# Optimization experiments

Measured on AMD Instinct MI355X. Metric: run time of the kernel, lower is better.

## Reference

```python
import jax, jax.numpy as jnp
import numpy as np

B = 32768   # batch (agents)
D = 2       # data_dim
E = 16      # embedding_dim
H = 128     # h_dim
M = 6       # num_modes
T = 30      # pred_len
EPS = 1e-5  # GroupNorm eps


def gn(x, w, b):
    # GroupNorm with 1 group over the last (channel) axis, per sample
    mu = x.mean(-1, keepdims=True)
    var = x.var(-1, keepdims=True)
    return (x - mu) * jax.lax.rsqrt(var + EPS) * w + b


def setup_inputs() -> dict:
    key = jax.random.key(0)
    ks = jax.random.split(key, 24)
    def n(k, shp, s=0.08):
        return jax.random.normal(k, shp, jnp.float32) * s
    return dict(
        last_obs=jax.random.normal(ks[0], (B, D), jnp.float32),
        last_obs_rel=jax.random.normal(ks[1], (B, D), jnp.float32),
        h0=jax.random.normal(ks[2], (B, H), jnp.float32),
        c0=jax.random.normal(ks[3], (B, H), jnp.float32),
        W_se=n(ks[4], (E, M * D)), b_se=n(ks[5], (E,)),
        W_ih=n(ks[6], (4 * H, E)), W_hh=n(ks[7], (4 * H, H)),
        b_ih=n(ks[8], (4 * H,)), b_hh=n(ks[9], (4 * H,)),
        mW1=n(ks[10], (M, H, H)), mg1w=jnp.ones((M, H)), mg1b=jnp.zeros((M, H)),
        mW2=n(ks[11], (M, H, H)), mg2w=jnp.ones((M, H)), mg2b=jnp.zeros((M, H)),
        mWo=n(ks[12], (M, H, D)), mbo=n(ks[13], (M, D)),
        cW1=n(ks[14], (H, H)), cg1w=jnp.ones((H,)), cg1b=jnp.zeros((H,)),
        cW2=n(ks[15], (H, H)), cg2w=jnp.ones((H,)), cg2b=jnp.zeros((H,)),
        cWo=n(ks[16], (H, M)), cbo=n(ks[17], (M,)),
    )


def reference(last_obs, last_obs_rel, h0, c0, W_se, b_se, W_ih, W_hh, b_ih, b_hh,
              mW1, mg1w, mg1b, mW2, mg2w, mg2b, mWo, mbo,
              cW1, cg1w, cg1b, cW2, cg2w, cg2b, cWo, cbo):
    assert last_obs.shape[1] == D
    # initial decoder input: last_obs_rel repeated over modes -> (B, M*D)
    x0 = jnp.tile(last_obs_rel, (1, M))
    dec_in = jax.nn.selu(x0 @ W_se.T + b_se)  # (B, E)

    def mode_heads(h):
        # six LinearRes(H,H,GN ng=1)+Linear(H,D) heads, batched over mode axis m
        t = jnp.einsum('bd,mde->mbe', h, mW1)
        t = jax.nn.relu(gn(t, mg1w[:, None, :], mg1b[:, None, :]))
        t = jnp.einsum('mbe,mef->mbf', t, mW2)
        t = gn(t, mg2w[:, None, :], mg2b[:, None, :])
        t = jax.nn.relu(t + h[None])
        out = jnp.einsum('mbf,mfo->mbo', t, mWo) + mbo[:, None, :]  # (M,B,D)
        return jnp.swapaxes(out, 0, 1)  # (B,M,D) -- cat over modes layout

    def step(carry, _):
        h, c, xin = carry
        g = xin @ W_ih.T + b_ih + h @ W_hh.T + b_hh  # (B, 4H), torch gate order i,f,g,o
        i, f, gg, o = jnp.split(g, 4, axis=-1)
        c = jax.nn.sigmoid(f) * c + jax.nn.sigmoid(i) * jnp.tanh(gg)
        h = jax.nn.sigmoid(o) * jnp.tanh(c)
        rel = mode_heads(h)  # (B,M,D)
        xin = jax.nn.selu(rel.reshape(rel.shape[0], M * D) @ W_se.T + b_se)
        return (h, c, xin), rel

    (hT, cT, _), rels = jax.lax.scan(step, (h0, c0, dec_in), None, length=T)
    pred = jnp.transpose(rels, (1, 2, 0, 3))  # (B, M, T, D)

    # confidence head: LinearRes + Linear(H, M) + softmax
    t = jax.nn.relu(gn(hT @ cW1, cg1w, cg1b))
    t = gn(t @ cW2, cg2w, cg2b)
    t = jax.nn.relu(t + hT)
    conf = jax.nn.softmax(t @ cWo + cbo, axis=1)  # (B, M)
    return pred, conf
```

## Files before the change

### kernel.cpp

```cpp
#include <hip/hip_runtime.h>
#include <hip/hip_bf16.h>
#include <cstdint>
#include <cstddef>


#define HD 128
#define TT 30
#define MM 6
#define B_ROWS 32768

typedef _Float16 f16x8 __attribute__((ext_vector_type(8)));
typedef _Float16 f16x4 __attribute__((ext_vector_type(4)));
typedef float f32x4 __attribute__((ext_vector_type(4)));

__device__ __forceinline__ float fast_rcp(float x) { return __builtin_amdgcn_rcpf(x); }
__device__ __forceinline__ float sigm(float x) { return fast_rcp(1.f + __expf(-x)); }
__device__ __forceinline__ float tanhf_(float x) { return 1.f - 2.f * fast_rcp(__expf(2.f * x) + 1.f); }
__device__ __forceinline__ float selu_(float x) {
  const float sc = 1.0507009873554805f;
  const float al = 1.6732632423543772f;
  return x > 0.f ? sc * x : sc * al * (__expf(x) - 1.f);
}

template <int CTRL>
__device__ __forceinline__ float dpp_add(float x) {
  union { float f; int i; } a, b;
  a.f = x;
  b.i = __builtin_amdgcn_update_dpp(a.i, a.i, CTRL, 0xF, 0xF, false);
  return x + b.f;
}
__device__ __forceinline__ float rowsum16(float x) {
  x = dpp_add<0x128>(x);
  x = dpp_add<0x124>(x);
  x = dpp_add<0x122>(x);
  x = dpp_add<0x121>(x);
  return x;
}
__device__ __forceinline__ f32x4 rowsum16x4(f32x4 v) {
  v[0] = rowsum16(v[0]); v[1] = rowsum16(v[1]);
  v[2] = rowsum16(v[2]); v[3] = rowsum16(v[3]);
  return v;
}

__global__ __launch_bounds__(256) void prep_weights(
    const float* __restrict__ W_ih, const float* __restrict__ W_hh,
    const float* __restrict__ b_ih, const float* __restrict__ b_hh,
    const float* __restrict__ mW1, const float* __restrict__ mW2,
    const float* __restrict__ cW1, const float* __restrict__ cW2,
    const float* __restrict__ mg1w, const float* __restrict__ mg1b,
    const float* __restrict__ mg2w, const float* __restrict__ mg2b,
    const float* __restrict__ mWo, const float* __restrict__ W_se,
    const float* __restrict__ b_se,
    _Float16* __restrict__ Wg, _Float16* __restrict__ W1p, _Float16* __restrict__ W2p,
    _Float16* __restrict__ cW1p, _Float16* __restrict__ cW2p, float* __restrict__ bg,
    float* __restrict__ ppA, float* __restrict__ ppB, float* __restrict__ ppC) {
  int n = blockIdx.x * 256 + threadIdx.x;
  if (n < 81920) {
    int t16 = n / 2560, r = n % 2560;
    int ch = r / 512, l = (r >> 3) & 63, j = r & 7;
    int q = l >> 4, cl = l & 15;
    int cg = t16 >> 2, g = t16 & 3;
    int row = g * 128 + cg * 16 + cl;
    int k = ch * 32 + q * 8 + j;
    float v = 0.f;
    if (k < 128) v = W_hh[row * 128 + k];
    else if (k < 144) v = W_ih[row * 16 + (k - 128)];
    Wg[n] = (_Float16)v;
    return;
  }
  n -= 81920;
  if (n < 98304) {
    int m = n >> 14, r = n & 16383;
    int ct = r >> 11, ch = (r >> 9) & 3, l = (r >> 3) & 63, j = r & 7;
    int q = l >> 4, cl = l & 15;
    int outcol = ct * 16 + cl, k = ch * 32 + q * 8 + j;
    W1p[n] = (_Float16)mW1[(m * 128 + k) * 128 + outcol];
    return;
  }
  n -= 98304;
  if (n < 98304) {
    int m = n >> 14, r = n & 16383;
    int ct = r >> 11, ch = (r >> 9) & 3, l = (r >> 3) & 63, j = r & 7;
    int q = l >> 4, cl = l & 15;
    int outcol = ct * 16 + cl, k = ch * 32 + q * 8 + j;
    W2p[n] = (_Float16)mW2[(m * 128 + k) * 128 + outcol];
    return;
  }
  n -= 98304;
  if (n < 16384) {
    int ct = n >> 11, ch = (n >> 9) & 3, l = (n >> 3) & 63, j = n & 7;
    int q = l >> 4, cl = l & 15;
    int outcol = ct * 16 + cl, k = ch * 32 + q * 8 + j;
    cW1p[n] = (_Float16)cW1[k * 128 + outcol];
    return;
  }
  n -= 16384;
  if (n < 16384) {
    int ct = n >> 11, ch = (n >> 9) & 3, l = (n >> 3) & 63, j = n & 7;
    int q = l >> 4, cl = l & 15;
    int outcol = ct * 16 + cl, k = ch * 32 + q * 8 + j;
    cW2p[n] = (_Float16)cW2[k * 128 + outcol];
    return;
  }
  n -= 16384;
  if (n < 512) { bg[n] = b_ih[n] + b_hh[n]; return; }
  n -= 512;
  if (n < 1536) {
    int m = n >> 8, r = n & 255;
    int cl = r >> 4, k = r & 15;
    float v = (k < 8) ? mg1w[m * 128 + k * 16 + cl] : mg1b[m * 128 + (k - 8) * 16 + cl];
    ppA[n] = v;
    return;
  }
  n -= 1536;
  if (n < 3072) {
    int m = n >> 9, r = n & 511;
    int cl = r >> 5, k = r & 31;
    int ct = k & 7, sel = k >> 3;
    float v;
    if (sel == 0)      v = mg2w[m * 128 + ct * 16 + cl];
    else if (sel == 1) v = mg2b[m * 128 + ct * 16 + cl];
    else               v = mWo[((size_t)m * 128 + ct * 16 + cl) * 2 + (sel - 2)];
    ppB[n] = v;
    return;
  }
  n -= 3072;
  if (n < 224) {
    int g = n / 56, k = n % 56;
    float v = 0.f;
    if (k < 48)      v = W_se[(g * 4 + k / 12) * 12 + (k % 12)];
    else if (k < 52) v = b_se[g * 4 + (k - 48)];
    ppC[n] = v;
    return;
  }
}

__device__ __forceinline__ void stage_chunk(int idx, _Float16* dst, int w, int lane,
                                            const _Float16* __restrict__ Wg,
                                            const _Float16* __restrict__ W1p,
                                            const _Float16* __restrict__ W2p) {
  const _Float16* src;
  int nblk;
  if (idx < 8) {
    src = Wg + idx * 10240;
    nblk = 20;
  } else {
    int j = idx - 8, m = j >> 2, r = j & 3;
    src = ((r & 2) ? W2p : W1p) + m * 16384 + (r & 1) * 8192;
    nblk = 16;
  }
  for (int i = w; i < nblk; i += 4) {
    __builtin_amdgcn_global_load_lds(
        (const __attribute__((address_space(1))) void*)(src + i * 512 + lane * 8),
        (__attribute__((address_space(3))) void*)(dst + i * 512 + lane * 8),
        16, 0, 0);
  }
}

__device__ __forceinline__ f32x4 mfma16(f16x8 a, f16x8 b, f32x4 c) {
  return __builtin_amdgcn_mfma_f32_16x16x32_f16(a, b, c, 0, 0, 0);
}

__device__ __forceinline__ void gemm_half(const f16x8 (&a)[4], const _Float16* buf,
                                          int lane, f32x4 (&acc)[8], int base) {
#pragma unroll
  for (int ctl = 0; ctl < 4; ++ctl) {
    const _Float16* bp = buf + ctl * 2048 + lane * 8;
    f32x4 a0 = {0.f, 0.f, 0.f, 0.f};
#pragma unroll
    for (int ch = 0; ch < 4; ++ch) {
      f16x8 b = *(const f16x8*)(bp + ch * 512);
      a0 = mfma16(a[ch], b, a0);
    }
    acc[base + ctl] = a0;
  }
}

__global__ __launch_bounds__(256, 2) void mmdec_main(
    const float* __restrict__ last_obs_rel, const float* __restrict__ h0, const float* __restrict__ c0,
    const float* __restrict__ mbo, const float* __restrict__ cg1w, const float* __restrict__ cg1b,
    const float* __restrict__ cg2w, const float* __restrict__ cg2b,
    const float* __restrict__ cWo, const float* __restrict__ cbo,
    const _Float16* __restrict__ Wg, const _Float16* __restrict__ W1p, const _Float16* __restrict__ W2p,
    const _Float16* __restrict__ cW1p, const _Float16* __restrict__ cW2p, const float* __restrict__ bgp,
    const float* __restrict__ ppA, const float* __restrict__ ppB, const float* __restrict__ ppC,
    float* __restrict__ out) {
  __shared__ __align__(16) unsigned char smem[81920];
  _Float16* stage0 = (_Float16*)smem;
  unsigned char* h_base = smem + 40960;
  unsigned char* t1_base = smem + 61440;
  float* rel_all = (float*)(smem + 78848);

  const int tid = threadIdx.x;
  const int w = tid >> 6;
  const int lane = tid & 63;
  const int q = lane >> 4, cl = lane & 15;
  const int rowbase = blockIdx.x * 64 + w * 16;

  auto hrow = [&](int r) -> _Float16* { return (_Float16*)(h_base + (w * 16 + r) * 320); };
  auto t1row = [&](int r) -> _Float16* { return (_Float16*)(t1_base + (w * 16 + r) * 272); };
  float* relw = rel_all + w * 16 * 12;

  auto sbuf = [&](int idx) -> _Float16* { return stage0 + ((idx & 1) ? 10240 : 0); };

  {
    const int rr = lane & 15, seg = lane >> 4;
    const float* src = h0 + (size_t)(rowbase + rr) * HD + seg * 32;
    _Float16* dst = hrow(rr) + seg * 32;
#pragma unroll
    for (int i = 0; i < 32; i += 8) {
      f32x4 a = *(const f32x4*)(src + i);
      f32x4 b = *(const f32x4*)(src + i + 4);
      f16x8 v;
#pragma unroll
      for (int k = 0; k < 4; ++k) { v[k] = (_Float16)a[k]; v[4 + k] = (_Float16)b[k]; }
      *(f16x8*)(dst + i) = v;
    }
    const float r0 = last_obs_rel[(size_t)(rowbase + rr) * 2 + 0];
    const float r1 = last_obs_rel[(size_t)(rowbase + rr) * 2 + 1];
    const int e0 = seg * 4;
    f16x4 v;
#pragma unroll
    for (int i = 0; i < 4; ++i) {
      const int e = e0 + i;
      float acc = ppC[seg * 56 + 48 + i];
#pragma unroll
      for (int j = 0; j < 12; ++j) acc += ((j & 1) ? r1 : r0) * ppC[seg * 56 + i * 12 + j];
      v[i] = (_Float16)selu_(acc);
    }
    *(f16x4*)(hrow(rr) + 128 + e0) = v;
    if (lane < 16) {
      f16x8 z;
#pragma unroll
      for (int i = 0; i < 8; ++i) z[i] = (_Float16)0.f;
      *(f16x8*)(hrow(lane) + 144) = z;
      *(f16x8*)(hrow(lane) + 152) = z;
    }
  }
  f32x4 cacc[8];
#pragma unroll
  for (int cg = 0; cg < 8; ++cg)
#pragma unroll
    for (int r = 0; r < 4; ++r)
      cacc[cg][r] = c0[(size_t)(rowbase + q * 4 + r) * HD + cg * 16 + cl];
  float bgh[8][4];
#pragma unroll
  for (int cg = 0; cg < 8; ++cg)
#pragma unroll
    for (int g = 0; g < 4; ++g) bgh[cg][g] = bgp[g * 128 + cg * 16 + cl];
  f32x4 hc[8];

  const int pA_ = lane, pB_ = 64 + lane;
  const size_t obA = ((size_t)(rowbase + pA_ / 6) * MM + pA_ % 6) * TT;
  const size_t obB = ((size_t)(rowbase + pB_ / 6) * MM + pB_ % 6) * TT;
  const int rlA = (pA_ / 6) * 12 + (pA_ % 6) * 2;
  const int rlB = (pB_ / 6) * 12 + (pB_ % 6) * 2;

  const float* wsp = ppC + (lane >> 4) * 56;

  stage_chunk(0, sbuf(0), w, lane, Wg, W1p, W2p);
  __syncthreads();

  const size_t confbase = (size_t)B_ROWS * MM * TT * 2;

  for (int t = 0; t < TT; ++t) {
    f16x8 afr[5];
#pragma unroll
    for (int ch = 0; ch < 5; ++ch)
      afr[ch] = *(const f16x8*)(hrow(cl) + ch * 32 + q * 8);

    for (int cg = 0; cg < 8; ++cg) {
      stage_chunk((cg + 1) & 31, sbuf(cg + 1), w, lane, Wg, W1p, W2p);
      const _Float16* buf = sbuf(cg);
      f32x4 gacc[4];
#pragma unroll
      for (int g = 0; g < 4; ++g) gacc[g] = f32x4{0.f, 0.f, 0.f, 0.f};
#pragma unroll
      for (int g = 0; g < 4; ++g) {
        const _Float16* bp = buf + g * 2560 + lane * 8;
#pragma unroll
        for (int ch = 0; ch < 5; ++ch) {
          f16x8 b = *(const f16x8*)(bp + ch * 512);
          gacc[g] = mfma16(afr[ch], b, gacc[g]);
        }
      }
#pragma unroll
      for (int r = 0; r < 4; ++r) {
        const float iv = sigm(gacc[0][r] + bgh[cg][0]);
        const float fv = sigm(gacc[1][r] + bgh[cg][1]);
        const float gv = tanhf_(gacc[2][r] + bgh[cg][2]);
        const float ov = sigm(gacc[3][r] + bgh[cg][3]);
        const float cn = fv * cacc[cg][r] + iv * gv;
        cacc[cg][r] = cn;
        const float hv = ov * tanhf_(cn);
        hc[cg][r] = hv;
        hrow(q * 4 + r)[cg * 16 + cl] = (_Float16)hv;
      }
      __syncthreads();
    }

    f16x8 frag[4];
#pragma unroll
    for (int ch = 0; ch < 4; ++ch)
      frag[ch] = *(const f16x8*)(hrow(cl) + ch * 32 + q * 8);

    for (int m = 0; m < MM; ++m) {
      const int base = 8 + m * 4;
      const float* pAv = ppA + (m * 16 + cl) * 16;
      const f32x4 g1wA = *(const f32x4*)(pAv);
      const f32x4 g1wB = *(const f32x4*)(pAv + 4);
      const f32x4 g1bA = *(const f32x4*)(pAv + 8);
      const f32x4 g1bB = *(const f32x4*)(pAv + 12);

      f32x4 acc1[8];
      stage_chunk((base + 1) & 31, sbuf(base + 1), w, lane, Wg, W1p, W2p);
      gemm_half(frag, sbuf(base), lane, acc1, 0);
      __syncthreads();
      stage_chunk((base + 2) & 31, sbuf(base + 2), w, lane, Wg, W1p, W2p);
      gemm_half(frag, sbuf(base + 1), lane, acc1, 4);
      f32x4 mean, rstd;
      {
        f32x4 s1 = {0.f, 0.f, 0.f, 0.f}, s2 = {0.f, 0.f, 0.f, 0.f};
#pragma unroll
        for (int ct = 0; ct < 8; ++ct) { s1 += acc1[ct]; s2 += acc1[ct] * acc1[ct]; }
        s1 = rowsum16x4(s1); s2 = rowsum16x4(s2);
        mean = s1 * (1.f / 128.f);
#pragma unroll
        for (int r = 0; r < 4; ++r)
          rstd[r] = rsqrtf(s2[r] * (1.f / 128.f) - mean[r] * mean[r] + 1e-5f);
      }
#pragma unroll
      for (int ct = 0; ct < 8; ++ct) {
        const float g1 = (ct < 4) ? g1wA[ct & 3] : g1wB[ct & 3];
        const float b1 = (ct < 4) ? g1bA[ct & 3] : g1bB[ct & 3];
#pragma unroll
        for (int r = 0; r < 4; ++r) {
          float v = (acc1[ct][r] - mean[r]) * rstd[r] * g1 + b1;
          t1row(q * 4 + r)[ct * 16 + cl] = (_Float16)fmaxf(v, 0.f);
        }
      }
      __syncthreads();
      const float* pBv = ppB + (m * 16 + cl) * 32;
      const f32x4 g2wA = *(const f32x4*)(pBv);
      const f32x4 g2wB = *(const f32x4*)(pBv + 4);
      const f32x4 g2bA = *(const f32x4*)(pBv + 8);
      const f32x4 g2bB = *(const f32x4*)(pBv + 12);
      const f32x4 w0A  = *(const f32x4*)(pBv + 16);
      const f32x4 w0B  = *(const f32x4*)(pBv + 20);
      const f32x4 w1A  = *(const f32x4*)(pBv + 24);
      const f32x4 w1B  = *(const f32x4*)(pBv + 28);
      f16x8 at1[4];
#pragma unroll
      for (int ch = 0; ch < 4; ++ch)
        at1[ch] = *(const f16x8*)(t1row(cl) + ch * 32 + q * 8);
      f32x4 acc2[8];
      stage_chunk((base + 3) & 31, sbuf(base + 3), w, lane, Wg, W1p, W2p);
      gemm_half(at1, sbuf(base + 2), lane, acc2, 0);
      __syncthreads();
      stage_chunk((base + 4) & 31, sbuf(base + 4), w, lane, Wg, W1p, W2p);
      gemm_half(at1, sbuf(base + 3), lane, acc2, 4);
      f32x4 mean2, rstd2;
      {
        f32x4 s1 = {0.f, 0.f, 0.f, 0.f}, s2 = {0.f, 0.f, 0.f, 0.f};
#pragma unroll
        for (int ct = 0; ct < 8; ++ct) { s1 += acc2[ct]; s2 += acc2[ct] * acc2[ct]; }
        s1 = rowsum16x4(s1); s2 = rowsum16x4(s2);
        mean2 = s1 * (1.f / 128.f);
#pragma unroll
        for (int r = 0; r < 4; ++r)
          rstd2[r] = rsqrtf(s2[r] * (1.f / 128.f) - mean2[r] * mean2[r] + 1e-5f);
      }
      f32x4 po0 = {0.f, 0.f, 0.f, 0.f}, po1 = {0.f, 0.f, 0.f, 0.f};
#pragma unroll
      for (int ct = 0; ct < 8; ++ct) {
        const float g2 = (ct < 4) ? g2wA[ct & 3] : g2wB[ct & 3];
        const float b2 = (ct < 4) ? g2bA[ct & 3] : g2bB[ct & 3];
        const float w0 = (ct < 4) ? w0A[ct & 3] : w0B[ct & 3];
        const float w1 = (ct < 4) ? w1A[ct & 3] : w1B[ct & 3];
#pragma unroll
        for (int r = 0; r < 4; ++r) {
          float v = (acc2[ct][r] - mean2[r]) * rstd2[r] * g2 + b2 + hc[ct][r];
          v = fmaxf(v, 0.f);
          po0[r] += v * w0;
          po1[r] += v * w1;
        }
      }
      po0 = rowsum16x4(po0);
      po1 = rowsum16x4(po1);
      if (cl < 2) {
#pragma unroll
        for (int r = 0; r < 4; ++r) {
          const int rl_ = q * 4 + r;
          relw[rl_ * 12 + m * 2 + cl] = (cl ? po1[r] : po0[r]) + mbo[m * 2 + cl];
        }
      }
      __syncthreads();
    }

    {
      float2 vA;
      vA.x = relw[rlA]; vA.y = relw[rlA + 1];
      *(float2*)(out + (obA + t) * 2) = vA;
      if (lane < 32) {
        float2 vB;
        vB.x = relw[rlB]; vB.y = relw[rlB + 1];
        *(float2*)(out + (obB + t) * 2) = vB;
      }
    }
    {
      const int rr = lane & 15;
      const f32x4 rl0 = *(const f32x4*)(relw + rr * 12);
      const f32x4 rl1 = *(const f32x4*)(relw + rr * 12 + 4);
      const f32x4 rl2 = *(const f32x4*)(relw + rr * 12 + 8);
      f32x4 wv0, wv1, wv2, bsv;
      bsv = *(const f32x4*)(wsp + 48);
      f16x4 v;
#pragma unroll
      for (int i = 0; i < 4; ++i) {
        wv0 = *(const f32x4*)(wsp + i * 12);
        wv1 = *(const f32x4*)(wsp + i * 12 + 4);
        wv2 = *(const f32x4*)(wsp + i * 12 + 8);
        float acc = bsv[i];
#pragma unroll
        for (int j = 0; j < 4; ++j) acc += rl0[j] * wv0[j];
#pragma unroll
        for (int j = 0; j < 4; ++j) acc += rl1[j] * wv1[j];
#pragma unroll
        for (int j = 0; j < 4; ++j) acc += rl2[j] * wv2[j];
        v[i] = (_Float16)selu_(acc);
      }
      *(f16x4*)(hrow(rr) + 128 + (lane >> 4) * 4) = v;
    }
  }

  {
    f16x8 frag[4];
#pragma unroll
    for (int ch = 0; ch < 4; ++ch)
      frag[ch] = *(const f16x8*)(hrow(cl) + ch * 32 + q * 8);
    f32x4 acc1[8];
#pragma unroll
    for (int ct = 0; ct < 8; ++ct) {
      const _Float16* bp = cW1p + ct * 2048 + lane * 8;
      f32x4 a0 = {0.f, 0.f, 0.f, 0.f};
#pragma unroll
      for (int ch = 0; ch < 4; ++ch) {
        f16x8 b = *(const f16x8*)(bp + ch * 512);
        a0 = mfma16(frag[ch], b, a0);
      }
      acc1[ct] = a0;
    }
    f32x4 mean, rstd;
    {
      f32x4 s1 = {0.f, 0.f, 0.f, 0.f}, s2 = {0.f, 0.f, 0.f, 0.f};
#pragma unroll
      for (int ct = 0; ct < 8; ++ct) { s1 += acc1[ct]; s2 += acc1[ct] * acc1[ct]; }
      s1 = rowsum16x4(s1); s2 = rowsum16x4(s2);
      mean = s1 * (1.f / 128.f);
#pragma unroll
      for (int r = 0; r < 4; ++r)
        rstd[r] = rsqrtf(s2[r] * (1.f / 128.f) - mean[r] * mean[r] + 1e-5f);
    }
#pragma unroll
    for (int ct = 0; ct < 8; ++ct) {
      const float g1 = cg1w[ct * 16 + cl];
      const float b1 = cg1b[ct * 16 + cl];
#pragma unroll
      for (int r = 0; r < 4; ++r) {
        float v = (acc1[ct][r] - mean[r]) * rstd[r] * g1 + b1;
        t1row(q * 4 + r)[ct * 16 + cl] = (_Float16)fmaxf(v, 0.f);
      }
    }
    f16x8 at1[4];
#pragma unroll
    for (int ch = 0; ch < 4; ++ch)
      at1[ch] = *(const f16x8*)(t1row(cl) + ch * 32 + q * 8);
    f32x4 acc2[8];
#pragma unroll
    for (int ct = 0; ct < 8; ++ct) {
      const _Float16* bp = cW2p + ct * 2048 + lane * 8;
      f32x4 a0 = {0.f, 0.f, 0.f, 0.f};
#pragma unroll
      for (int ch = 0; ch < 4; ++ch) {
        f16x8 b = *(const f16x8*)(bp + ch * 512);
        a0 = mfma16(at1[ch], b, a0);
      }
      acc2[ct] = a0;
    }
    f32x4 mean2, rstd2;
    {
      f32x4 s1 = {0.f, 0.f, 0.f, 0.f}, s2 = {0.f, 0.f, 0.f, 0.f};
#pragma unroll
      for (int ct = 0; ct < 8; ++ct) { s1 += acc2[ct]; s2 += acc2[ct] * acc2[ct]; }
      s1 = rowsum16x4(s1); s2 = rowsum16x4(s2);
      mean2 = s1 * (1.f / 128.f);
#pragma unroll
      for (int r = 0; r < 4; ++r)
        rstd2[r] = rsqrtf(s2[r] * (1.f / 128.f) - mean2[r] * mean2[r] + 1e-5f);
    }
    float pl[4][6];
#pragma unroll
    for (int r = 0; r < 4; ++r)
#pragma unroll
      for (int k = 0; k < 6; ++k) pl[r][k] = 0.f;
#pragma unroll
    for (int ct = 0; ct < 8; ++ct) {
      const float g2 = cg2w[ct * 16 + cl];
      const float b2 = cg2b[ct * 16 + cl];
      float wo[6];
#pragma unroll
      for (int k = 0; k < 6; ++k) wo[k] = cWo[(ct * 16 + cl) * 6 + k];
#pragma unroll
      for (int r = 0; r < 4; ++r) {
        float v = (acc2[ct][r] - mean2[r]) * rstd2[r] * g2 + b2 + hc[ct][r];
        v = fmaxf(v, 0.f);
#pragma unroll
        for (int k = 0; k < 6; ++k) pl[r][k] += v * wo[k];
      }
    }
#pragma unroll
    for (int r = 0; r < 4; ++r)
#pragma unroll
      for (int k = 0; k < 6; ++k) pl[r][k] = rowsum16(pl[r][k]);
    if (cl == 0) {
#pragma unroll
      for (int r = 0; r < 4; ++r) {
        float l[6];
#pragma unroll
        for (int k = 0; k < 6; ++k) l[k] = pl[r][k] + cbo[k];
        float mx = l[0];
#pragma unroll
        for (int k = 1; k < 6; ++k) mx = fmaxf(mx, l[k]);
        float s = 0.f;
#pragma unroll
        for (int k = 0; k < 6; ++k) { l[k] = __expf(l[k] - mx); s += l[k]; }
        const float inv = fast_rcp(s);
#pragma unroll
        for (int k = 0; k < 6; ++k)
          out[confbase + (size_t)(rowbase + q * 4 + r) * 6 + k] = l[k] * inv;
      }
    }
  }
}

extern "C" void kernel_launch(void* const* d_in, const int* in_sizes, int n_in,
                              void* d_out, int out_size, void* d_ws, size_t ws_size,
                              hipStream_t stream) {
  (void)in_sizes; (void)n_in; (void)out_size; (void)ws_size;
  const float* last_obs_rel = (const float*)d_in[1];
  const float* h0   = (const float*)d_in[2];
  const float* c0   = (const float*)d_in[3];
  const float* W_se = (const float*)d_in[4];
  const float* b_se = (const float*)d_in[5];
  const float* W_ih = (const float*)d_in[6];
  const float* W_hh = (const float*)d_in[7];
  const float* b_ih = (const float*)d_in[8];
  const float* b_hh = (const float*)d_in[9];
  const float* mW1  = (const float*)d_in[10];
  const float* mg1w = (const float*)d_in[11];
  const float* mg1b = (const float*)d_in[12];
  const float* mW2  = (const float*)d_in[13];
  const float* mg2w = (const float*)d_in[14];
  const float* mg2b = (const float*)d_in[15];
  const float* mWo  = (const float*)d_in[16];
  const float* mbo  = (const float*)d_in[17];
  const float* cW1  = (const float*)d_in[18];
  const float* cg1w = (const float*)d_in[19];
  const float* cg1b = (const float*)d_in[20];
  const float* cW2  = (const float*)d_in[21];
  const float* cg2w = (const float*)d_in[22];
  const float* cg2b = (const float*)d_in[23];
  const float* cWo  = (const float*)d_in[24];
  const float* cbo  = (const float*)d_in[25];

  char* ws = (char*)d_ws;
  _Float16* Wg   = (_Float16*)(ws + 0);
  _Float16* W1p  = (_Float16*)(ws + 163840);
  _Float16* W2p  = (_Float16*)(ws + 360448);
  _Float16* cW1p = (_Float16*)(ws + 557056);
  _Float16* cW2p = (_Float16*)(ws + 589824);
  float*    bg   = (float*)   (ws + 622592);
  float*    ppA  = (float*)   (ws + 624640);
  float*    ppB  = (float*)   (ws + 630784);
  float*    ppC  = (float*)   (ws + 643072);

  prep_weights<<<1237, 256, 0, stream>>>(W_ih, W_hh, b_ih, b_hh, mW1, mW2, cW1, cW2,
                                         mg1w, mg1b, mg2w, mg2b, mWo, W_se, b_se,
                                         Wg, W1p, W2p, cW1p, cW2p, bg, ppA, ppB, ppC);
  mmdec_main<<<B_ROWS / 64, 256, 0, stream>>>(last_obs_rel, h0, c0,
                                              mbo, cg1w, cg1b, cg2w, cg2b, cWo, cbo,
                                              Wg, W1p, W2p, cW1p, cW2p, bg,
                                              ppA, ppB, ppC, (float*)d_out);
}
```

Measured before the change: 1.703 ms.

## Deepen weight staging to 4-slot ring with prefetch distance two and finer barriers

Replaces the double-buffered 20KB weight chunks with a 4-slot ring of half-size chunks, prefetched two chunks ahead via global_load_lds. Each chunk advance uses explicit vmcnt/lgkmcnt waits and a raw s_barrier in place of __syncthreads, and several separate __syncthreads are removed. The aim is more latency hiding for weight streaming and shorter barrier stalls, at the cost of twice as many barriers per step and fragile hand-tuned wait counts.

```diff
diff --git a/kernel.cpp b/kernel.cpp
--- a/kernel.cpp
+++ b/kernel.cpp
@@ -135,45 +135,8 @@
   }
 }
 
-__device__ __forceinline__ void stage_chunk(int idx, _Float16* dst, int w, int lane,
-                                            const _Float16* __restrict__ Wg,
-                                            const _Float16* __restrict__ W1p,
-                                            const _Float16* __restrict__ W2p) {
-  const _Float16* src;
-  int nblk;
-  if (idx < 8) {
-    src = Wg + idx * 10240;
-    nblk = 20;
-  } else {
-    int j = idx - 8, m = j >> 2, r = j & 3;
-    src = ((r & 2) ? W2p : W1p) + m * 16384 + (r & 1) * 8192;
-    nblk = 16;
-  }
-  for (int i = w; i < nblk; i += 4) {
-    __builtin_amdgcn_global_load_lds(
-        (const __attribute__((address_space(1))) void*)(src + i * 512 + lane * 8),
-        (__attribute__((address_space(3))) void*)(dst + i * 512 + lane * 8),
-        16, 0, 0);
-  }
-}
-
 __device__ __forceinline__ f32x4 mfma16(f16x8 a, f16x8 b, f32x4 c) {
   return __builtin_amdgcn_mfma_f32_16x16x32_f16(a, b, c, 0, 0, 0);
-}
-
-__device__ __forceinline__ void gemm_half(const f16x8 (&a)[4], const _Float16* buf,
-                                          int lane, f32x4 (&acc)[8], int base) {
-#pragma unroll
-  for (int ctl = 0; ctl < 4; ++ctl) {
-    const _Float16* bp = buf + ctl * 2048 + lane * 8;
-    f32x4 a0 = {0.f, 0.f, 0.f, 0.f};
-#pragma unroll
-    for (int ch = 0; ch < 4; ++ch) {
-      f16x8 b = *(const f16x8*)(bp + ch * 512);
-      a0 = mfma16(a[ch], b, a0);
-    }
-    acc[base + ctl] = a0;
-  }
 }
 
 __global__ __launch_bounds__(256, 2) void mmdec_main(
@@ -201,7 +164,41 @@
   auto t1row = [&](int r) -> _Float16* { return (_Float16*)(t1_base + (w * 16 + r) * 272); };
   float* relw = rel_all + w * 16 * 12;
 
-  auto sbuf = [&](int idx) -> _Float16* { return stage0 + ((idx & 1) ? 10240 : 0); };
+  auto gll = [&](const _Float16* s, _Float16* d) {
+    __builtin_amdgcn_global_load_lds(
+        (const __attribute__((address_space(1))) void*)s,
+        (__attribute__((address_space(3))) void*)d, 16, 0, 0);
+  };
+  auto stage_chunk = [&](int c) {
+    const _Float16* src;
+    int nblk;
+    if (c < 16) {
+      src = Wg + c * 5120;
+      nblk = 10;
+    } else {
+      const int j = c - 16, m = j >> 3, r = j & 7;
+      src = ((r & 4) ? W2p : W1p) + m * 16384 + (r & 3) * 4096;
+      nblk = 8;
+    }
+    _Float16* dst = stage0 + (c & 3) * 5120;
+    for (int i = w; i < nblk; i += 4)
+      gll(src + i * 512 + lane * 8, dst + i * 512 + lane * 8);
+  };
+  auto ADV = [&](int c) {
+    asm volatile("s_waitcnt lgkmcnt(0)" ::: "memory");
+    __builtin_amdgcn_sched_barrier(0);
+    stage_chunk((c + 2) & 63);
+    if (w < 2) {
+      if (c <= 13 || c == 63) asm volatile("s_waitcnt vmcnt(6)" ::: "memory");
+      else if (c == 14 || c == 62) asm volatile("s_waitcnt vmcnt(5)" ::: "memory");
+      else asm volatile("s_waitcnt vmcnt(4)" ::: "memory");
+    } else {
+      asm volatile("s_waitcnt vmcnt(4)" ::: "memory");
+    }
+    __builtin_amdgcn_sched_barrier(0);
+    __builtin_amdgcn_s_barrier();
+    __builtin_amdgcn_sched_barrier(0);
+  };
 
   {
     const int rr = lane & 15, seg = lane >> 4;
@@ -222,7 +219,6 @@
     f16x4 v;
 #pragma unroll
     for (int i = 0; i < 4; ++i) {
-      const int e = e0 + i;
       float acc = ppC[seg * 56 + 48 + i];
 #pragma unroll
       for (int j = 0; j < 12; ++j) acc += ((j & 1) ? r1 : r0) * ppC[seg * 56 + i * 12 + j];
@@ -258,31 +254,37 @@
 
   const float* wsp = ppC + (lane >> 4) * 56;
 
-  stage_chunk(0, sbuf(0), w, lane, Wg, W1p, W2p);
+  stage_chunk(0);
+  stage_chunk(1);
   __syncthreads();
 
   const size_t confbase = (size_t)B_ROWS * MM * TT * 2;
 
   for (int t = 0; t < TT; ++t) {
+    int c = 0;
     f16x8 afr[5];
 #pragma unroll
     for (int ch = 0; ch < 5; ++ch)
       afr[ch] = *(const f16x8*)(hrow(cl) + ch * 32 + q * 8);
 
     for (int cg = 0; cg < 8; ++cg) {
-      stage_chunk((cg + 1) & 31, sbuf(cg + 1), w, lane, Wg, W1p, W2p);
-      const _Float16* buf = sbuf(cg);
       f32x4 gacc[4];
 #pragma unroll
       for (int g = 0; g < 4; ++g) gacc[g] = f32x4{0.f, 0.f, 0.f, 0.f};
 #pragma unroll
-      for (int g = 0; g < 4; ++g) {
-        const _Float16* bp = buf + g * 2560 + lane * 8;
-#pragma unroll
-        for (int ch = 0; ch < 5; ++ch) {
-          f16x8 b = *(const f16x8*)(bp + ch * 512);
-          gacc[g] = mfma16(afr[ch], b, gacc[g]);
+      for (int half = 0; half < 2; ++half) {
+        ADV(c);
+        const _Float16* slot = stage0 + (c & 3) * 5120;
+#pragma unroll
+        for (int gl = 0; gl < 2; ++gl) {
+          const _Float16* bp = slot + gl * 2560 + lane * 8;
+#pragma unroll
+          for (int ch = 0; ch < 5; ++ch) {
+            f16x8 b = *(const f16x8*)(bp + ch * 512);
+            gacc[half * 2 + gl] = mfma16(afr[ch], b, gacc[half * 2 + gl]);
+          }
         }
+        ++c;
       }
 #pragma unroll
       for (int r = 0; r < 4; ++r) {
@@ -296,7 +298,6 @@
         hc[cg][r] = hv;
         hrow(q * 4 + r)[cg * 16 + cl] = (_Float16)hv;
       }
-      __syncthreads();
     }
 
     f16x8 frag[4];
@@ -305,7 +306,6 @@
       frag[ch] = *(const f16x8*)(hrow(cl) + ch * 32 + q * 8);
 
     for (int m = 0; m < MM; ++m) {
-      const int base = 8 + m * 4;
       const float* pAv = ppA + (m * 16 + cl) * 16;
       const f32x4 g1wA = *(const f32x4*)(pAv);
       const f32x4 g1wB = *(const f32x4*)(pAv + 4);
@@ -313,11 +313,23 @@
       const f32x4 g1bB = *(const f32x4*)(pAv + 12);
 
       f32x4 acc1[8];
-      stage_chunk((base + 1) & 31, sbuf(base + 1), w, lane, Wg, W1p, W2p);
-      gemm_half(frag, sbuf(base), lane, acc1, 0);
-      __syncthreads();
-      stage_chunk((base + 2) & 31, sbuf(base + 2), w, lane, Wg, W1p, W2p);
-      gemm_half(frag, sbuf(base + 1), lane, acc1, 4);
+#pragma unroll
+      for (int qh = 0; qh < 4; ++qh) {
+        ADV(c);
+        const _Float16* slot = stage0 + (c & 3) * 5120;
+#pragma unroll
+        for (int ctl = 0; ctl < 2; ++ctl) {
+          const _Float16* bp = slot + ctl * 2048 + lane * 8;
+          f32x4 a0 = {0.f, 0.f, 0.f, 0.f};
+#pragma unroll
+          for (int ch = 0; ch < 4; ++ch) {
+            f16x8 b = *(const f16x8*)(bp + ch * 512);
+            a0 = mfma16(frag[ch], b, a0);
+          }
+          acc1[qh * 2 + ctl] = a0;
+        }
+        ++c;
+      }
       f32x4 mean, rstd;
       {
         f32x4 s1 = {0.f, 0.f, 0.f, 0.f}, s2 = {0.f, 0.f, 0.f, 0.f};
@@ -339,7 +351,6 @@
           t1row(q * 4 + r)[ct * 16 + cl] = (_Float16)fmaxf(v, 0.f);
         }
       }
-      __syncthreads();
       const float* pBv = ppB + (m * 16 + cl) * 32;
       const f32x4 g2wA = *(const f32x4*)(pBv);
       const f32x4 g2wB = *(const f32x4*)(pBv + 4);
@@ -354,11 +365,23 @@
       for (int ch = 0; ch < 4; ++ch)
         at1[ch] = *(const f16x8*)(t1row(cl) + ch * 32 + q * 8);
       f32x4 acc2[8];
-      stage_chunk((base + 3) & 31, sbuf(base + 3), w, lane, Wg, W1p, W2p);
-      gemm_half(at1, sbuf(base + 2), lane, acc2, 0);
-      __syncthreads();
-      stage_chunk((base + 4) & 31, sbuf(base + 4), w, lane, Wg, W1p, W2p);
-      gemm_half(at1, sbuf(base + 3), lane, acc2, 4);
+#pragma unroll
+      for (int qh = 0; qh < 4; ++qh) {
+        ADV(c);
+        const _Float16* slot = stage0 + (c & 3) * 5120;
+#pragma unroll
+        for (int ctl = 0; ctl < 2; ++ctl) {
+          const _Float16* bp = slot + ctl * 2048 + lane * 8;
+          f32x4 a0 = {0.f, 0.f, 0.f, 0.f};
+#pragma unroll
+          for (int ch = 0; ch < 4; ++ch) {
+            f16x8 b = *(const f16x8*)(bp + ch * 512);
+            a0 = mfma16(at1[ch], b, a0);
+          }
+          acc2[qh * 2 + ctl] = a0;
+        }
+        ++c;
+      }
       f32x4 mean2, rstd2;
       {
         f32x4 s1 = {0.f, 0.f, 0.f, 0.f}, s2 = {0.f, 0.f, 0.f, 0.f};
@@ -394,7 +417,6 @@
           relw[rl_ * 12 + m * 2 + cl] = (cl ? po1[r] : po0[r]) + mbo[m * 2 + cl];
         }
       }
-      __syncthreads();
     }
 
     {
```

Result: no change. 1.709 ms (+0.4%).

## Software-pipeline LSTM and GN2 epilogues behind next MFMA block, raise MFMA priority

Applied to the files above, without the earlier changes.

Restructures the LSTM gate loop so the MFMA for gate chunk cg is issued before the sigmoid/tanh epilogue of chunk cg-1, and defers each mode's GN2/output-projection epilogue into the next mode's first GEMM half. Wraps MFMA sections in s_setprio(1) so the matrix work gets issue priority over other waves' VALU epilogues. The intent is to overlap transcendental/VALU epilogue work with matrix-core work across the two resident blocks. It costs extra live registers (previous gate accumulators and a 32-float acc2 copy) under launch_bounds(256,2), which could cause spilling.

```diff
diff --git a/kernel.cpp b/kernel.cpp
--- a/kernel.cpp
+++ b/kernel.cpp
@@ -163,6 +163,7 @@
 
 __device__ __forceinline__ void gemm_half(const f16x8 (&a)[4], const _Float16* buf,
                                           int lane, f32x4 (&acc)[8], int base) {
+  __builtin_amdgcn_s_setprio(1);
 #pragma unroll
   for (int ctl = 0; ctl < 4; ++ctl) {
     const _Float16* bp = buf + ctl * 2048 + lane * 8;
@@ -174,6 +175,7 @@
     }
     acc[base + ctl] = a0;
   }
+  __builtin_amdgcn_s_setprio(0);
 }
 
 __global__ __launch_bounds__(256, 2) void mmdec_main(
@@ -222,7 +224,6 @@
     f16x4 v;
 #pragma unroll
     for (int i = 0; i < 4; ++i) {
-      const int e = e0 + i;
       float acc = ppC[seg * 56 + 48 + i];
 #pragma unroll
       for (int j = 0; j < 12; ++j) acc += ((j & 1) ? r1 : r0) * ppC[seg * 56 + i * 12 + j];
@@ -258,6 +259,68 @@
 
   const float* wsp = ppC + (lane >> 4) * 56;
 
+  auto lstm_epi = [&](int cgi, const f32x4 (&gg)[4]) {
+#pragma unroll
+    for (int r = 0; r < 4; ++r) {
+      const float iv = sigm(gg[0][r] + bgh[cgi][0]);
+      const float fv = sigm(gg[1][r] + bgh[cgi][1]);
+      const float gv = tanhf_(gg[2][r] + bgh[cgi][2]);
+      const float ov = sigm(gg[3][r] + bgh[cgi][3]);
+      const float cn = fv * cacc[cgi][r] + iv * gv;
+      cacc[cgi][r] = cn;
+      const float hv = ov * tanhf_(cn);
+      hc[cgi][r] = hv;
+      hrow(q * 4 + r)[cgi * 16 + cl] = (_Float16)hv;
+    }
+  };
+
+  auto gn2_epi = [&](int mi, const f32x4 (&a2)[8]) {
+    const float* pBv = ppB + (mi * 16 + cl) * 32;
+    const f32x4 g2wA = *(const f32x4*)(pBv);
+    const f32x4 g2wB = *(const f32x4*)(pBv + 4);
+    const f32x4 g2bA = *(const f32x4*)(pBv + 8);
+    const f32x4 g2bB = *(const f32x4*)(pBv + 12);
+    const f32x4 w0A  = *(const f32x4*)(pBv + 16);
+    const f32x4 w0B  = *(const f32x4*)(pBv + 20);
+    const f32x4 w1A  = *(const f32x4*)(pBv + 24);
+    const f32x4 w1B  = *(const f32x4*)(pBv + 28);
+    f32x4 mean2, rstd2;
+    {
+      f32x4 s1 = {0.f, 0.f, 0.f, 0.f}, s2 = {0.f, 0.f, 0.f, 0.f};
+#pragma unroll
+      for (int ct = 0; ct < 8; ++ct) { s1 += a2[ct]; s2 += a2[ct] * a2[ct]; }
+      s1 = rowsum16x4(s1); s2 = rowsum16x4(s2);
+      mean2 = s1 * (1.f / 128.f);
+#pragma unroll
+      for (int r = 0; r < 4; ++r)
+        rstd2[r] = rsqrtf(s2[r] * (1.f / 128.f) - mean2[r] * mean2[r] + 1e-5f);
+    }
+    f32x4 po0 = {0.f, 0.f, 0.f, 0.f}, po1 = {0.f, 0.f, 0.f, 0.f};
+#pragma unroll
+    for (int ct = 0; ct < 8; ++ct) {
+      const float g2 = (ct < 4) ? g2wA[ct & 3] : g2wB[ct & 3];
+      const float b2 = (ct < 4) ? g2bA[ct & 3] : g2bB[ct & 3];
+      const float w0 = (ct < 4) ? w0A[ct & 3] : w0B[ct & 3];
+      const float w1 = (ct < 4) ? w1A[ct & 3] : w1B[ct & 3];
+#pragma unroll
+      for (int r = 0; r < 4; ++r) {
+        float v = (a2[ct][r] - mean2[r]) * rstd2[r] * g2 + b2 + hc[ct][r];
+        v = fmaxf(v, 0.f);
+        po0[r] += v * w0;
+        po1[r] += v * w1;
+      }
+    }
+    po0 = rowsum16x4(po0);
+    po1 = rowsum16x4(po1);
+    if (cl < 2) {
+#pragma unroll
+      for (int r = 0; r < 4; ++r) {
+        const int rl_ = q * 4 + r;
+        relw[rl_ * 12 + mi * 2 + cl] = (cl ? po1[r] : po0[r]) + mbo[mi * 2 + cl];
+      }
+    }
+  };
+
   stage_chunk(0, sbuf(0), w, lane, Wg, W1p, W2p);
   __syncthreads();
 
@@ -269,41 +332,55 @@
     for (int ch = 0; ch < 5; ++ch)
       afr[ch] = *(const f16x8*)(hrow(cl) + ch * 32 + q * 8);
 
-    for (int cg = 0; cg < 8; ++cg) {
+    f32x4 gp[4];
+    {
+      stage_chunk(1, sbuf(1), w, lane, Wg, W1p, W2p);
+      const _Float16* buf = sbuf(0);
+      __builtin_amdgcn_s_setprio(1);
+#pragma unroll
+      for (int g = 0; g < 4; ++g) {
+        const _Float16* bp = buf + g * 2560 + lane * 8;
+        f32x4 a = {0.f, 0.f, 0.f, 0.f};
+#pragma unroll
+        for (int ch = 0; ch < 5; ++ch) {
+          f16x8 b = *(const f16x8*)(bp + ch * 512);
+          a = mfma16(afr[ch], b, a);
+        }
+        gp[g] = a;
+      }
+      __builtin_amdgcn_s_setprio(0);
+      __syncthreads();
+    }
+    for (int cg = 1; cg < 8; ++cg) {
       stage_chunk((cg + 1) & 31, sbuf(cg + 1), w, lane, Wg, W1p, W2p);
       const _Float16* buf = sbuf(cg);
-      f32x4 gacc[4];
-#pragma unroll
-      for (int g = 0; g < 4; ++g) gacc[g] = f32x4{0.f, 0.f, 0.f, 0.f};
+      f32x4 gc[4];
+      __builtin_amdgcn_s_setprio(1);
 #pragma unroll
       for (int g = 0; g < 4; ++g) {
         const _Float16* bp = buf + g * 2560 + lane * 8;
+        f32x4 a = {0.f, 0.f, 0.f, 0.f};
 #pragma unroll
         for (int ch = 0; ch < 5; ++ch) {
           f16x8 b = *(const f16x8*)(bp + ch * 512);
-          gacc[g] = mfma16(afr[ch], b, gacc[g]);
+          a = mfma16(afr[ch], b, a);
         }
-      }
-#pragma unroll
-      for (int r = 0; r < 4; ++r) {
-        const float iv = sigm(gacc[0][r] + bgh[cg][0]);
-        const float fv = sigm(gacc[1][r] + bgh[cg][1]);
-        const float gv = tanhf_(gacc[2][r] + bgh[cg][2]);
-        const float ov = sigm(gacc[3][r] + bgh[cg][3]);
-        const float cn = fv * cacc[cg][r] + iv * gv;
-        cacc[cg][r] = cn;
-        const float hv = ov * tanhf_(cn);
-        hc[cg][r] = hv;
-        hrow(q * 4 + r)[cg * 16 + cl] = (_Float16)hv;
-      }
+        gc[g] = a;
+      }
+      __builtin_amdgcn_s_setprio(0);
+      lstm_epi(cg - 1, gp);
+#pragma unroll
+      for (int g = 0; g < 4; ++g) gp[g] = gc[g];
       __syncthreads();
     }
+    lstm_epi(7, gp);
 
     f16x8 frag[4];
 #pragma unroll
     for (int ch = 0; ch < 4; ++ch)
       frag[ch] = *(const f16x8*)(hrow(cl) + ch * 32 + q * 8);
 
+    f32x4 a2p[8];
     for (int m = 0; m < MM; ++m) {
       const int base = 8 + m * 4;
       const float* pAv = ppA + (m * 16 + cl) * 16;
@@ -315,6 +392,7 @@
       f32x4 acc1[8];
       stage_chunk((base + 1) & 31, sbuf(base + 1), w, lane, Wg, W1p, W2p);
       gemm_half(frag, sbuf(base), lane, acc1, 0);
+      if (m > 0) gn2_epi(m - 1, a2p);
       __syncthreads();
       stage_chunk((base + 2) & 31, sbuf(base + 2), w, lane, Wg, W1p, W2p);
       gemm_half(frag, sbuf(base + 1), lane, acc1, 4);
@@ -340,15 +418,6 @@
         }
       }
       __syncthreads();
-      const float* pBv = ppB + (m * 16 + cl) * 32;
-      const f32x4 g2wA = *(const f32x4*)(pBv);
-      const f32x4 g2wB = *(const f32x4*)(pBv + 4);
-      const f32x4 g2bA = *(const f32x4*)(pBv + 8);
-      const f32x4 g2bB = *(const f32x4*)(pBv + 12);
-      const f32x4 w0A  = *(const f32x4*)(pBv + 16);
-      const f32x4 w0B  = *(const f32x4*)(pBv + 20);
-      const f32x4 w1A  = *(const f32x4*)(pBv + 24);
-      const f32x4 w1B  = *(const f32x4*)(pBv + 28);
       f16x8 at1[4];
 #pragma unroll
       for (int ch = 0; ch < 4; ++ch)
@@ -359,43 +428,11 @@
       __syncthreads();
       stage_chunk((base + 4) & 31, sbuf(base + 4), w, lane, Wg, W1p, W2p);
       gemm_half(at1, sbuf(base + 3), lane, acc2, 4);
-      f32x4 mean2, rstd2;
-      {
-        f32x4 s1 = {0.f, 0.f, 0.f, 0.f}, s2 = {0.f, 0.f, 0.f, 0.f};
-#pragma unroll
-        for (int ct = 0; ct < 8; ++ct) { s1 += acc2[ct]; s2 += acc2[ct] * acc2[ct]; }
-        s1 = rowsum16x4(s1); s2 = rowsum16x4(s2);
-        mean2 = s1 * (1.f / 128.f);
-#pragma unroll
-        for (int r = 0; r < 4; ++r)
-          rstd2[r] = rsqrtf(s2[r] * (1.f / 128.f) - mean2[r] * mean2[r] + 1e-5f);
-      }
-      f32x4 po0 = {0.f, 0.f, 0.f, 0.f}, po1 = {0.f, 0.f, 0.f, 0.f};
-#pragma unroll
-      for (int ct = 0; ct < 8; ++ct) {
-        const float g2 = (ct < 4) ? g2wA[ct & 3] : g2wB[ct & 3];
-        const float b2 = (ct < 4) ? g2bA[ct & 3] : g2bB[ct & 3];
-        const float w0 = (ct < 4) ? w0A[ct & 3] : w0B[ct & 3];
-        const float w1 = (ct < 4) ? w1A[ct & 3] : w1B[ct & 3];
-#pragma unroll
-        for (int r = 0; r < 4; ++r) {
-          float v = (acc2[ct][r] - mean2[r]) * rstd2[r] * g2 + b2 + hc[ct][r];
-          v = fmaxf(v, 0.f);
-          po0[r] += v * w0;
-          po1[r] += v * w1;
-        }
-      }
-      po0 = rowsum16x4(po0);
-      po1 = rowsum16x4(po1);
-      if (cl < 2) {
-#pragma unroll
-        for (int r = 0; r < 4; ++r) {
-          const int rl_ = q * 4 + r;
-          relw[rl_ * 12 + m * 2 + cl] = (cl ? po1[r] : po0[r]) + mbo[m * 2 + cl];
-        }
-      }
+#pragma unroll
+      for (int ct = 0; ct < 8; ++ct) a2p[ct] = acc2[ct];
       __syncthreads();
     }
+    gn2_epi(5, a2p);
 
     {
       float2 vA;
```

Result: slower. 1.969 ms (+15.6%).
